# Kernel tuning notes

Measured on AMD Instinct MI355X. Metric: run time of the kernel, lower is better.

Reference implementation:

```python
import jax, jax.numpy as jnp
import numpy as np
import math

B, S, D, H, DFF, L = 8, 1024, 512, 8, 2048, 4
DK = D // H
EPS = 1e-5
NEG = -1e32


def _sinusoidal_pe(s, d):
    pos = np.arange(s)[:, None].astype(np.float32)
    div = np.exp(np.arange(0, d, 2).astype(np.float32) * (-math.log(10000.0) / d))
    pe = np.zeros((s, d), np.float32)
    pe[:, 0::2] = np.sin(pos * div)
    pe[:, 1::2] = np.cos(pos * div)
    return jnp.asarray(pe)


def setup_inputs() -> dict:
    key = jax.random.key(0)
    ks = jax.random.split(key, 20)
    sd = 0.02
    inp = {
        "q_embed_data": jax.random.normal(ks[0], (B, S, D), jnp.float32),
        "qa_embed_data": jax.random.normal(ks[1], (B, S, D), jnp.float32),
        "pe": _sinusoidal_pe(S, D),
        # stacked per-layer params (leading dim L). kq_same=1 -> q uses Wk.
        "Wk": sd * jax.random.normal(ks[2], (L, D, D), jnp.float32),
        "bk": jnp.zeros((L, D), jnp.float32),
        "Wv": sd * jax.random.normal(ks[3], (L, D, D), jnp.float32),
        "bv": jnp.zeros((L, D), jnp.float32),
        "Wo": sd * jax.random.normal(ks[4], (L, D, D), jnp.float32),
        "bo": jnp.zeros((L, D), jnp.float32),
        "ln1_s": jnp.ones((L, D), jnp.float32),
        "ln1_b": jnp.zeros((L, D), jnp.float32),
        "W1": sd * jax.random.normal(ks[5], (L, D, DFF), jnp.float32),
        "b1": jnp.zeros((L, DFF), jnp.float32),
        "W2": sd * jax.random.normal(ks[6], (L, DFF, D), jnp.float32),
        "b2": jnp.zeros((L, D), jnp.float32),
        "ln2_s": jnp.ones((L, D), jnp.float32),
        "ln2_b": jnp.zeros((L, D), jnp.float32),
    }
    return inp


def _layernorm(z, s, b):
    m = z.mean(-1, keepdims=True)
    v = ((z - m) ** 2).mean(-1, keepdims=True)
    return (z - m) / jnp.sqrt(v + EPS) * s + b


def _forward(q_embed_data, qa_embed_data, pe, Wk, bk, Wv, bv, Wo, bo,
             ln1_s, ln1_b, W1, b1, W2, b2, ln2_s, ln2_b):
    x = q_embed_data + pe[None, :, :]
    y = qa_embed_data + pe[None, :, :]  # values source stays fixed across blocks
    allowed = jnp.tril(jnp.ones((S, S), bool), -1)  # strictly-causal: attend only to j < i
    row_keep = (jnp.arange(S) > 0).astype(x.dtype)[None, None, :, None]  # zero_pad row 0

    def heads(z, W, b):
        return (z @ W + b).reshape(B, S, H, DK).transpose(0, 2, 1, 3)  # [B,H,S,DK]

    def step(xc, p):
        wk, bk_, wv, bv_, wo, bo_, s1, b1n, w1, b1f, w2, b2f, s2, b2n = p
        q = heads(xc, wk, bk_)  # kq_same: q via k_linear
        k = heads(xc, wk, bk_)
        v = heads(y, wv, bv_)
        sc = jnp.einsum('bhid,bhjd->bhij', q, k) / math.sqrt(DK)
        att = jax.nn.softmax(jnp.where(allowed, sc, NEG), axis=-1) * row_keep
        o = jnp.einsum('bhij,bhjd->bhid', att, v).transpose(0, 2, 1, 3).reshape(B, S, D)
        x1 = _layernorm(xc + (o @ wo + bo_), s1, b1n)
        f = jax.nn.relu(x1 @ w1 + b1f) @ w2 + b2f
        x2 = _layernorm(x1 + f, s2, b2n)
        return x2, None

    out, _ = jax.lax.scan(step, x, (Wk, bk, Wv, bv, Wo, bo, ln1_s, ln1_b, W1, b1, W2, b2, ln2_s, ln2_b))
    return out


def reference(q_embed_data, qa_embed_data, pe, Wk, bk, Wv, bv, Wo, bo,
              ln1_s, ln1_b, W1, b1, W2, b2, ln2_s, ln2_b):
    return _forward(q_embed_data, qa_embed_data, pe, Wk, bk, Wv, bv, Wo, bo,
                    ln1_s, ln1_b, W1, b1, W2, b2, ln2_s, ln2_b)
```

## Files before the change

kernel.cpp:

```cpp
#include <hip/hip_runtime.h>
#include <stdint.h>

typedef __attribute__((ext_vector_type(8))) __bf16 bf16x8;
typedef __attribute__((ext_vector_type(4))) float f32x4;
typedef __attribute__((ext_vector_type(4))) unsigned int u32x4;

constexpr int B = 8, S = 1024, D = 512, H = 8, DFF = 2048, L = 4, DK = 64;
constexpr int MR = B * S;

__device__ __forceinline__ unsigned short f2bf(float f) {
    union { float f; unsigned u; } v; v.f = f;
    unsigned u = v.u;
    u += 0x7fffu + ((u >> 16) & 1u);
    return (unsigned short)(u >> 16);
}

__device__ __forceinline__ void gload_lds16(const void* g, void* l) {
    __builtin_amdgcn_global_load_lds(
        (const __attribute__((address_space(1))) void*)g,
        (__attribute__((address_space(3))) void*)l, 16, 0, 0);
}

__global__ __launch_bounds__(256) void add_pe_kernel(
    const float* __restrict__ qe, const float* __restrict__ qa,
    const float* __restrict__ pe, float* __restrict__ x_f32,
    unsigned short* __restrict__ x_bf, unsigned short* __restrict__ y_bf) {
    int gid = blockIdx.x * 256 + threadIdx.x;
    int base = gid * 4;
    int po = base & (S * D - 1);
    float4 p = *(const float4*)(pe + po);
    float4 a = *(const float4*)(qe + base);
    float4 q = *(const float4*)(qa + base);
    float4 xv = make_float4(a.x + p.x, a.y + p.y, a.z + p.z, a.w + p.w);
    float4 yv = make_float4(q.x + p.x, q.y + p.y, q.z + p.z, q.w + p.w);
    *(float4*)(x_f32 + base) = xv;
    ushort4 xb; xb.x = f2bf(xv.x); xb.y = f2bf(xv.y); xb.z = f2bf(xv.z); xb.w = f2bf(xv.w);
    ushort4 yb; yb.x = f2bf(yv.x); yb.y = f2bf(yv.y); yb.z = f2bf(yv.z); yb.w = f2bf(yv.w);
    *(ushort4*)(x_bf + base) = xb;
    *(ushort4*)(y_bf + base) = yb;
}

__global__ __launch_bounds__(256) void wtrans_kernel(
    const float* __restrict__ src, unsigned short* __restrict__ dst, int K, int N) {
    __shared__ float t[64][65];
    src += (size_t)blockIdx.z * K * N;
    dst += (size_t)blockIdx.z * K * N;
    int n0 = blockIdx.x * 64, k0 = blockIdx.y * 64;
    int tid = threadIdx.x;
    int r = tid >> 4, c4 = (tid & 15) * 4;
    #pragma unroll
    for (int rr = 0; rr < 64; rr += 16) {
        float4 v = *(const float4*)(src + (size_t)(k0 + r + rr) * N + n0 + c4);
        t[r + rr][c4] = v.x; t[r + rr][c4 + 1] = v.y;
        t[r + rr][c4 + 2] = v.z; t[r + rr][c4 + 3] = v.w;
    }
    __syncthreads();
    int n = tid >> 2, kc = (tid & 3) * 16;
    ushort4 o[4];
    #pragma unroll
    for (int g = 0; g < 4; g++) {
        o[g].x = f2bf(t[kc + g * 4 + 0][n]);
        o[g].y = f2bf(t[kc + g * 4 + 1][n]);
        o[g].z = f2bf(t[kc + g * 4 + 2][n]);
        o[g].w = f2bf(t[kc + g * 4 + 3][n]);
    }
    unsigned short* dp = dst + (size_t)(n0 + n) * K + k0 + kc;
    #pragma unroll
    for (int g = 0; g < 4; g++) *(ushort4*)(dp + g * 4) = o[g];
}

template<int BN, bool RELU, bool RESID, bool OUT_F32, bool OUT_BF16, bool OUT_VT, bool BOUNCE>
__global__ __launch_bounds__(256) void gemm_kernel(
    const unsigned short* __restrict__ A, const unsigned short* __restrict__ Bt,
    const float* __restrict__ bias, const float* __restrict__ resid,
    float* __restrict__ out_f32, unsigned short* __restrict__ out_bf,
    int M, int N, int K) {
    constexpr int MT = (BN == 128) ? 4 : 2;
    constexpr int WROWS = (BN == 128) ? 64 : 32;
    constexpr int BRND = (BN == 128) ? 4 : 2;
    __shared__ unsigned short lds[(128 + BN) * 64];
    unsigned short* a_lds = lds;
    unsigned short* b_lds = lds + 128 * 64;

    const int tid = threadIdx.x;
    const int lane = tid & 63, wid = tid >> 6;
    const int wm = (BN == 128) ? (wid >> 1) : wid;
    const int wn = (BN == 128) ? (wid & 1) : 0;
    const int l15 = lane & 15, quad = lane >> 4;
    const int nmt = gridDim.x, nnt = gridDim.y;
    const int o_lin = blockIdx.y * nmt + blockIdx.x;
    const int xcd = o_lin & 7, oi = o_lin >> 3;
    const int mtile = xcd * (nmt >> 3) + oi / nnt;
    const int ntile = oi % nnt;
    const int m0 = mtile * 128, n0 = ntile * BN;

    f32x4 acc[MT][4];
    #pragma unroll
    for (int i = 0; i < MT; i++)
        #pragma unroll
        for (int j = 0; j < 4; j++) { f32x4 z = {0.f, 0.f, 0.f, 0.f}; acc[i][j] = z; }

    const unsigned short* aP[4];
    unsigned short* aL[4];
    #pragma unroll
    for (int j = 0; j < 4; j++) {
        int c = wid * 256 + j * 64 + lane;
        int r = c >> 3, slot = c & 7, kg = slot ^ (r & 7);
        aP[j] = A + (size_t)(m0 + r) * K + kg * 8;
        aL[j] = a_lds + (size_t)(wid * 256 + j * 64) * 8;
    }
    const unsigned short* bP[BRND];
    unsigned short* bL[BRND];
    #pragma unroll
    for (int j = 0; j < BRND; j++) {
        int c = wid * (BRND * 64) + j * 64 + lane;
        int r = c >> 3, slot = c & 7, kg = slot ^ (r & 7);
        bP[j] = Bt + (size_t)(n0 + r) * K + kg * 8;
        bL[j] = b_lds + (size_t)(wid * (BRND * 64) + j * 64) * 8;
    }

    for (int k0 = 0; k0 < K; k0 += 64) {
        #pragma unroll
        for (int j = 0; j < 4; j++) gload_lds16(aP[j] + k0, aL[j]);
        #pragma unroll
        for (int j = 0; j < BRND; j++) gload_lds16(bP[j] + k0, bL[j]);
        __syncthreads();

        bf16x8 af[MT][2], bfv[4][2];
        #pragma unroll
        for (int mt = 0; mt < MT; mt++) {
            int row = wm * WROWS + mt * 16 + l15;
            #pragma unroll
            for (int kh = 0; kh < 2; kh++)
                af[mt][kh] = *(const bf16x8*)&a_lds[row * 64 + (((kh * 4 + quad) ^ (row & 7)) * 8)];
        }
        #pragma unroll
        for (int nt = 0; nt < 4; nt++) {
            int row = wn * 64 + nt * 16 + l15;
            #pragma unroll
            for (int kh = 0; kh < 2; kh++)
                bfv[nt][kh] = *(const bf16x8*)&b_lds[row * 64 + (((kh * 4 + quad) ^ (row & 7)) * 8)];
        }
        #pragma unroll
        for (int mt = 0; mt < MT; mt++)
            #pragma unroll
            for (int nt = 0; nt < 4; nt++) {
                acc[mt][nt] = __builtin_amdgcn_mfma_f32_16x16x32_bf16(af[mt][0], bfv[nt][0], acc[mt][nt], 0, 0, 0);
                acc[mt][nt] = __builtin_amdgcn_mfma_f32_16x16x32_bf16(af[mt][1], bfv[nt][1], acc[mt][nt], 0, 0, 0);
            }
        __syncthreads();
    }

    if constexpr (BOUNCE) {
        float* sc = (float*)lds + wid * (16 * 68);
        const int cbase = n0 + wn * 64;
        const int r2 = lane >> 2;
        const int c2 = (lane & 3) * 16;
        float4 bvv[4];
        #pragma unroll
        for (int i = 0; i < 4; i++) bvv[i] = *(const float4*)(bias + cbase + c2 + i * 4);
        #pragma unroll
        for (int mt = 0; mt < MT; mt++) {
            #pragma unroll
            for (int nt = 0; nt < 4; nt++)
                #pragma unroll
                for (int r = 0; r < 4; r++)
                    sc[(quad * 4 + r) * 68 + nt * 16 + l15] = acc[mt][nt][r];
            const int row_g = m0 + wm * WROWS + mt * 16 + r2;
            float v[16];
            #pragma unroll
            for (int i = 0; i < 4; i++) {
                float4 t = *(const float4*)&sc[r2 * 68 + c2 + i * 4];
                v[i * 4 + 0] = t.x + bvv[i].x; v[i * 4 + 1] = t.y + bvv[i].y;
                v[i * 4 + 2] = t.z + bvv[i].z; v[i * 4 + 3] = t.w + bvv[i].w;
            }
            if (RELU) {
                #pragma unroll
                for (int i = 0; i < 16; i++) v[i] = fmaxf(v[i], 0.f);
            }
            unsigned short ob[16];
            #pragma unroll
            for (int i = 0; i < 16; i++) ob[i] = f2bf(v[i]);
            unsigned short* op = out_bf + (size_t)row_g * N + cbase + c2;
            *(u32x4*)op = *(const u32x4*)ob;
            *(u32x4*)(op + 8) = *(const u32x4*)(ob + 8);
        }
    } else {
        #pragma unroll
        for (int nt = 0; nt < 4; nt++) {
            int col = n0 + wn * 64 + nt * 16 + l15;
            float bv = bias[col];
            #pragma unroll
            for (int mt = 0; mt < MT; mt++) {
                int row0 = m0 + wm * WROWS + mt * 16 + quad * 4;
                if (OUT_VT) {
                    int hh = col >> 6, d = col & 63;
                    int bb = row0 >> 10, s0 = row0 & 1023;
                    ushort4 o;
                    o.x = f2bf(acc[mt][nt][0] + bv);
                    o.y = f2bf(acc[mt][nt][1] + bv);
                    o.z = f2bf(acc[mt][nt][2] + bv);
                    o.w = f2bf(acc[mt][nt][3] + bv);
                    *(ushort4*)(out_bf + ((size_t)(bb * H + hh) * DK + d) * S + s0) = o;
                } else {
                    #pragma unroll
                    for (int r = 0; r < 4; r++) {
                        int row = row0 + r;
                        float v = acc[mt][nt][r] + bv;
                        if (RESID) v += resid[(size_t)row * N + col];
                        if (RELU) v = fmaxf(v, 0.f);
                        size_t o = (size_t)row * N + col;
                        if (OUT_F32) out_f32[o] = v;
                        if (OUT_BF16) out_bf[o] = f2bf(v);
                    }
                }
            }
        }
    }
}

__global__ __launch_bounds__(256) void gemm_qkv_kernel(
    const unsigned short* __restrict__ x_bf, const unsigned short* __restrict__ y_bf,
    const unsigned short* __restrict__ wkT, const unsigned short* __restrict__ wvT,
    const float* __restrict__ bk, const float* __restrict__ bv,
    unsigned short* __restrict__ qk_out, unsigned short* __restrict__ vt_out) {
    constexpr int BN = 64, MT = 2, WROWS = 32, BRND = 2;
    constexpr int N = 512, K = 512;
    __shared__ unsigned short a_lds[128 * 64];
    __shared__ unsigned short b_lds[BN * 64];

    const bool isv = blockIdx.z != 0;
    const unsigned short* A  = isv ? y_bf : x_bf;
    const unsigned short* Bt = isv ? wvT : wkT;
    const float* bias        = isv ? bv : bk;

    const int tid = threadIdx.x;
    const int lane = tid & 63, wid = tid >> 6;
    const int l15 = lane & 15, quad = lane >> 4;
    const int nmt = gridDim.x, nnt = gridDim.y;
    const int o_lin = blockIdx.y * nmt + blockIdx.x;
    const int xcd = o_lin & 7, oi = o_lin >> 3;
    const int mtile = xcd * (nmt >> 3) + oi / nnt;
    const int ntile = oi % nnt;
    const int m0 = mtile * 128, n0 = ntile * BN;

    f32x4 acc[MT][4];
    #pragma unroll
    for (int i = 0; i < MT; i++)
        #pragma unroll
        for (int j = 0; j < 4; j++) { f32x4 z = {0.f, 0.f, 0.f, 0.f}; acc[i][j] = z; }

    const unsigned short* aP[4];
    unsigned short* aL[4];
    #pragma unroll
    for (int j = 0; j < 4; j++) {
        int c = wid * 256 + j * 64 + lane;
        int r = c >> 3, slot = c & 7, kg = slot ^ (r & 7);
        aP[j] = A + (size_t)(m0 + r) * K + kg * 8;
        aL[j] = a_lds + (size_t)(wid * 256 + j * 64) * 8;
    }
    const unsigned short* bP[BRND];
    unsigned short* bL[BRND];
    #pragma unroll
    for (int j = 0; j < BRND; j++) {
        int c = wid * (BRND * 64) + j * 64 + lane;
        int r = c >> 3, slot = c & 7, kg = slot ^ (r & 7);
        bP[j] = Bt + (size_t)(n0 + r) * K + kg * 8;
        bL[j] = b_lds + (size_t)(wid * (BRND * 64) + j * 64) * 8;
    }

    for (int k0 = 0; k0 < K; k0 += 64) {
        #pragma unroll
        for (int j = 0; j < 4; j++) gload_lds16(aP[j] + k0, aL[j]);
        #pragma unroll
        for (int j = 0; j < BRND; j++) gload_lds16(bP[j] + k0, bL[j]);
        __syncthreads();

        bf16x8 af[MT][2], bfv[4][2];
        #pragma unroll
        for (int mt = 0; mt < MT; mt++) {
            int row = wid * WROWS + mt * 16 + l15;
            #pragma unroll
            for (int kh = 0; kh < 2; kh++)
                af[mt][kh] = *(const bf16x8*)&a_lds[row * 64 + (((kh * 4 + quad) ^ (row & 7)) * 8)];
        }
        #pragma unroll
        for (int nt = 0; nt < 4; nt++) {
            int row = nt * 16 + l15;
            #pragma unroll
            for (int kh = 0; kh < 2; kh++)
                bfv[nt][kh] = *(const bf16x8*)&b_lds[row * 64 + (((kh * 4 + quad) ^ (row & 7)) * 8)];
        }
        #pragma unroll
        for (int mt = 0; mt < MT; mt++)
            #pragma unroll
            for (int nt = 0; nt < 4; nt++) {
                acc[mt][nt] = __builtin_amdgcn_mfma_f32_16x16x32_bf16(af[mt][0], bfv[nt][0], acc[mt][nt], 0, 0, 0);
                acc[mt][nt] = __builtin_amdgcn_mfma_f32_16x16x32_bf16(af[mt][1], bfv[nt][1], acc[mt][nt], 0, 0, 0);
            }
        __syncthreads();
    }

    #pragma unroll
    for (int nt = 0; nt < 4; nt++) {
        int col = n0 + nt * 16 + l15;
        float bv_ = bias[col];
        #pragma unroll
        for (int mt = 0; mt < MT; mt++) {
            int row0 = m0 + wid * WROWS + mt * 16 + quad * 4;
            ushort4 o;
            o.x = f2bf(acc[mt][nt][0] + bv_);
            o.y = f2bf(acc[mt][nt][1] + bv_);
            o.z = f2bf(acc[mt][nt][2] + bv_);
            o.w = f2bf(acc[mt][nt][3] + bv_);
            if (isv) {
                int hh = col >> 6, d = col & 63;
                int bb = row0 >> 10, s0 = row0 & 1023;
                *(ushort4*)(vt_out + ((size_t)(bb * H + hh) * DK + d) * S + s0) = o;
            } else {
                #pragma unroll
                for (int r = 0; r < 4; r++)
                    qk_out[(size_t)(row0 + r) * N + col] =
                        (r == 0) ? o.x : (r == 1) ? o.y : (r == 2) ? o.z : o.w;
            }
        }
    }
}

__global__ __launch_bounds__(256) void ln_kernel(
    const float* __restrict__ in, const float* __restrict__ gamma,
    const float* __restrict__ beta, float* __restrict__ out_f32,
    unsigned short* __restrict__ out_bf) {
    __shared__ float red[8];
    int row = blockIdx.x, tid = threadIdx.x;
    const float* p = in + (size_t)row * D;
    float2 v = *(const float2*)(p + tid * 2);
    float s = v.x + v.y;
    float q = v.x * v.x + v.y * v.y;
    #pragma unroll
    for (int off = 32; off > 0; off >>= 1) {
        s += __shfl_xor(s, off);
        q += __shfl_xor(q, off);
    }
    int wid = tid >> 6, lane = tid & 63;
    if (lane == 0) { red[wid] = s; red[4 + wid] = q; }
    __syncthreads();
    s = red[0] + red[1] + red[2] + red[3];
    q = red[4] + red[5] + red[6] + red[7];
    float mean = s * (1.f / D);
    float var = q * (1.f / D) - mean * mean;
    float inv = rsqrtf(var + 1e-5f);
    int c = tid * 2;
    float2 g = *(const float2*)(gamma + c);
    float2 bb = *(const float2*)(beta + c);
    float o0 = (v.x - mean) * inv * g.x + bb.x;
    float o1 = (v.y - mean) * inv * g.y + bb.y;
    *(float2*)(out_f32 + (size_t)row * D + c) = make_float2(o0, o1);
    ushort2 ob; ob.x = f2bf(o0); ob.y = f2bf(o1);
    *(ushort2*)(out_bf + (size_t)row * D + c) = ob;
}

__global__ __launch_bounds__(256, 2) void attn_kernel(
    const unsigned short* __restrict__ qk, const unsigned short* __restrict__ vt,
    unsigned short* __restrict__ ob) {
    __shared__ unsigned short kbuf[2][64 * 64];
    __shared__ unsigned short vbuf[2][64 * 64];
    __shared__ unsigned p_u32[4][32 * 36];
    constexpr float C = 0.18033688011112042f;
    const float NEGINF = -__builtin_huge_valf();

    const int bx = blockIdx.x;
    const int Qb = 7 - (bx >> 6);
    const int hh = bx & 63;
    const int b = hh >> 3, h = hh & 7;
    const int head = hh;
    const int tid = threadIdx.x;
    const int w = tid >> 6, lane = tid & 63;
    const int l15 = lane & 15, quad = lane >> 4;

    const int nkt = 2 * Qb + 2;
    const int qrow0 = Qb * 128 + w * 32;

    const int rowbase = b * S, colbase = h * DK;
    const unsigned short* kbase = qk + (size_t)rowbase * D + colbase;
    const unsigned short* vbase = vt + (size_t)head * (DK * S);

    bf16x8 qf[2][2];
    #pragma unroll
    for (int u = 0; u < 2; u++) {
        const unsigned short* qrow =
            qk + (size_t)(rowbase + qrow0 + u * 16 + l15) * D + colbase;
        qf[u][0] = *(const bf16x8*)(qrow + quad * 8);
        qf[u][1] = *(const bf16x8*)(qrow + 32 + quad * 8);
    }

    const int sr = lane >> 3;
    const int sseg = (lane & 7) ^ sr;
    const unsigned short* kgp[2]; const unsigned short* vgp[2];
    unsigned short* kld[2]; unsigned short* vld[2];
    #pragma unroll
    for (int j = 0; j < 2; j++) {
        int rt = w * 16 + j * 8 + sr;
        kgp[j] = kbase + (size_t)rt * D + sseg * 8;
        vgp[j] = vbase + (size_t)rt * S + sseg * 8;
        kld[j] = &kbuf[0][(w * 16 + j * 8) * 64];
        vld[j] = &vbuf[0][(w * 16 + j * 8) * 64];
    }
    auto stage = [&](int buf, int kt) {
        #pragma unroll
        for (int j = 0; j < 2; j++) gload_lds16(kgp[j] + (size_t)kt * 64 * D, kld[j] + buf * 4096);
        #pragma unroll
        for (int j = 0; j < 2; j++) gload_lds16(vgp[j] + kt * 64, vld[j] + buf * 4096);
    };

    float l_r[2] = {0.f, 0.f};
    f32x4 o_acc[2][4];
    #pragma unroll
    for (int u = 0; u < 2; u++)
        #pragma unroll
        for (int i = 0; i < 4; i++) { f32x4 z = {0.f, 0.f, 0.f, 0.f}; o_acc[u][i] = z; }

    auto consume = [&](int kt, const unsigned short* kl, const unsigned short* vl) {
        unsigned* pb = p_u32[w];
        bf16x8 kf[4][2];
        #pragma unroll
        for (int mt = 0; mt < 4; mt++) {
            const unsigned short* kr = kl + (mt * 16 + l15) * 64;
            #pragma unroll
            for (int kh = 0; kh < 2; kh++)
                kf[mt][kh] = *(const bf16x8*)(kr + (((kh * 4 + quad) ^ (l15 & 7)) * 8));
        }
        const bool diag = kt * 64 + 64 > qrow0;
        #pragma unroll
        for (int u = 0; u < 2; u++) {
            const int qb = qrow0 + u * 16;
            const int ql = u * 16 + l15;
            #pragma unroll
            for (int mt = 0; mt < 4; mt++) {
                if (kt * 64 + mt * 16 < qb + 16) {
                    f32x4 a = {0.f, 0.f, 0.f, 0.f};
                    a = __builtin_amdgcn_mfma_f32_16x16x32_bf16(kf[mt][0], qf[u][0], a, 0, 0, 0);
                    a = __builtin_amdgcn_mfma_f32_16x16x32_bf16(kf[mt][1], qf[u][1], a, 0, 0, 0);
                    if (diag) {
                        const int gi = qb + l15;
                        #pragma unroll
                        for (int r = 0; r < 4; r++) {
                            int gj = kt * 64 + mt * 16 + quad * 4 + r;
                            a[r] = (gj >= gi) ? NEGINF : a[r];
                        }
                    }
                    float e0 = exp2f(a[0] * C), e1 = exp2f(a[1] * C);
                    float e2 = exp2f(a[2] * C), e3 = exp2f(a[3] * C);
                    unsigned pk0, pk1;
                    asm("v_cvt_pk_bf16_f32 %0, %1, %2" : "=v"(pk0) : "v"(e0), "v"(e1));
                    asm("v_cvt_pk_bf16_f32 %0, %1, %2" : "=v"(pk1) : "v"(e2), "v"(e3));
                    l_r[u] += (e0 + e1) + (e2 + e3);
                    *(uint2*)&pb[ql * 36 + mt * 8 + quad * 2] = make_uint2(pk0, pk1);
                } else {
                    *(uint2*)&pb[ql * 36 + mt * 8 + quad * 2] = make_uint2(0u, 0u);
                }
            }
        }
        bf16x8 vf[4][2];
        #pragma unroll
        for (int mt = 0; mt < 4; mt++) {
            const unsigned short* vr = vl + (mt * 16 + l15) * 64;
            #pragma unroll
            for (int kh = 0; kh < 2; kh++)
                vf[mt][kh] = *(const bf16x8*)(vr + (((kh * 4 + quad) ^ (l15 & 7)) * 8));
        }
        #pragma unroll
        for (int u = 0; u < 2; u++) {
            const int qb = qrow0 + u * 16;
            const int ql = u * 16 + l15;
            u32x4 d0 = *(const u32x4*)&pb[ql * 36 + quad * 4];
            bf16x8 pb0 = __builtin_bit_cast(bf16x8, d0);
            const bool hi = (kt * 64 + 32 < qb + 16);
            if (hi) {
                u32x4 d1 = *(const u32x4*)&pb[ql * 36 + 16 + quad * 4];
                bf16x8 pb1 = __builtin_bit_cast(bf16x8, d1);
                #pragma unroll
                for (int mt = 0; mt < 4; mt++) {
                    o_acc[u][mt] = __builtin_amdgcn_mfma_f32_16x16x32_bf16(vf[mt][0], pb0, o_acc[u][mt], 0, 0, 0);
                    o_acc[u][mt] = __builtin_amdgcn_mfma_f32_16x16x32_bf16(vf[mt][1], pb1, o_acc[u][mt], 0, 0, 0);
                }
            } else {
                #pragma unroll
                for (int mt = 0; mt < 4; mt++)
                    o_acc[u][mt] = __builtin_amdgcn_mfma_f32_16x16x32_bf16(vf[mt][0], pb0, o_acc[u][mt], 0, 0, 0);
            }
        }
    };

    stage(0, 0);
    for (int kt = 0; kt < nkt; ++kt) {
        const int cur = kt & 1;
        if (kt + 1 < nkt) {
            stage(cur ^ 1, kt + 1);
            asm volatile("s_waitcnt vmcnt(4)" ::: "memory");
        } else {
            asm volatile("s_waitcnt vmcnt(0)" ::: "memory");
        }
        __builtin_amdgcn_sched_barrier(0);
        __builtin_amdgcn_s_barrier();
        __builtin_amdgcn_sched_barrier(0);
        if (kt * 64 < qrow0 + 32)
            consume(kt, &kbuf[cur][0], &vbuf[cur][0]);
        __builtin_amdgcn_sched_barrier(0);
        __builtin_amdgcn_s_barrier();
        __builtin_amdgcn_sched_barrier(0);
    }

    #pragma unroll
    for (int u = 0; u < 2; u++) {
        l_r[u] += __shfl_xor(l_r[u], 16);
        l_r[u] += __shfl_xor(l_r[u], 32);
    }
    #pragma unroll
    for (int u = 0; u < 2; u++) {
        const int si = qrow0 + u * 16 + l15;
        float inv = (l_r[u] > 0.f) ? 1.f / l_r[u] : 0.f;
        if (si == 0) inv = 0.f;
        unsigned short* orow = ob + (size_t)(b * S + si) * D + h * DK;
        #pragma unroll
        for (int mt = 0; mt < 4; mt++) {
            ushort4 o;
            o.x = f2bf(o_acc[u][mt][0] * inv);
            o.y = f2bf(o_acc[u][mt][1] * inv);
            o.z = f2bf(o_acc[u][mt][2] * inv);
            o.w = f2bf(o_acc[u][mt][3] * inv);
            *(ushort4*)(orow + mt * 16 + quad * 4) = o;
        }
    }
}

extern "C" void kernel_launch(void* const* d_in, const int* in_sizes, int n_in,
                              void* d_out, int out_size, void* d_ws, size_t ws_size,
                              hipStream_t stream) {
    (void)in_sizes; (void)n_in; (void)out_size; (void)ws_size;
    const float* qe  = (const float*)d_in[0];
    const float* qa  = (const float*)d_in[1];
    const float* pe  = (const float*)d_in[2];
    const float* Wk  = (const float*)d_in[3];
    const float* bk  = (const float*)d_in[4];
    const float* Wv  = (const float*)d_in[5];
    const float* bv  = (const float*)d_in[6];
    const float* Wo  = (const float*)d_in[7];
    const float* bo  = (const float*)d_in[8];
    const float* l1s = (const float*)d_in[9];
    const float* l1b = (const float*)d_in[10];
    const float* W1  = (const float*)d_in[11];
    const float* b1  = (const float*)d_in[12];
    const float* W2  = (const float*)d_in[13];
    const float* b2  = (const float*)d_in[14];
    const float* l2s = (const float*)d_in[15];
    const float* l2b = (const float*)d_in[16];

    char* w = (char*)d_ws;
    float* x_f32  = (float*)w;           w += (size_t)MR * D * 4;
    float* t_f32  = (float*)w;           w += (size_t)MR * D * 4;
    float* x1_f32 = (float*)w;           w += (size_t)MR * D * 4;
    unsigned short* x_bf  = (unsigned short*)w; w += (size_t)MR * D * 2;
    unsigned short* y_bf  = (unsigned short*)w; w += (size_t)MR * D * 2;
    unsigned short* qk_bf = (unsigned short*)w; w += (size_t)MR * D * 2;
    unsigned short* vt_bf = (unsigned short*)w; w += (size_t)MR * D * 2;
    unsigned short* o_bf  = (unsigned short*)w; w += (size_t)MR * D * 2;
    unsigned short* x1_bf = (unsigned short*)w; w += (size_t)MR * D * 2;
    unsigned short* h_bf  = (unsigned short*)w; w += (size_t)MR * DFF * 2;
    unsigned short* wkT = (unsigned short*)w;   w += (size_t)L * D * D * 2;
    unsigned short* wvT = (unsigned short*)w;   w += (size_t)L * D * D * 2;
    unsigned short* woT = (unsigned short*)w;   w += (size_t)L * D * D * 2;
    unsigned short* w1T = (unsigned short*)w;   w += (size_t)L * D * DFF * 2;
    unsigned short* w2T = (unsigned short*)w;   w += (size_t)L * DFF * D * 2;

    add_pe_kernel<<<MR * D / 4 / 256, 256, 0, stream>>>(qe, qa, pe, x_f32, x_bf, y_bf);
    wtrans_kernel<<<dim3(8, 8, L), 256, 0, stream>>>(Wk, wkT, D, D);
    wtrans_kernel<<<dim3(8, 8, L), 256, 0, stream>>>(Wv, wvT, D, D);
    wtrans_kernel<<<dim3(8, 8, L), 256, 0, stream>>>(Wo, woT, D, D);
    wtrans_kernel<<<dim3(32, 8, L), 256, 0, stream>>>(W1, w1T, D, DFF);
    wtrans_kernel<<<dim3(8, 32, L), 256, 0, stream>>>(W2, w2T, DFF, D);

    dim3 g512(64, 8), g2048(64, 16);
    for (int l = 0; l < L; l++) {
        gemm_qkv_kernel<<<dim3(64, 8, 2), 256, 0, stream>>>(
            x_bf, y_bf, wkT + (size_t)l * D * D, wvT + (size_t)l * D * D,
            bk + l * D, bv + l * D, qk_bf, vt_bf);
        attn_kernel<<<512, 256, 0, stream>>>(qk_bf, vt_bf, o_bf);
        gemm_kernel<64, false, true, true, false, false, false><<<g512, 256, 0, stream>>>(
            o_bf, woT + (size_t)l * D * D, bo + l * D, x_f32, t_f32, nullptr, MR, D, D);
        ln_kernel<<<MR, 256, 0, stream>>>(t_f32, l1s + l * D, l1b + l * D, x1_f32, x1_bf);
        gemm_kernel<128, true, false, false, true, false, true><<<g2048, 256, 0, stream>>>(
            x1_bf, w1T + (size_t)l * D * DFF, b1 + l * DFF, nullptr, nullptr, h_bf, MR, DFF, D);
        gemm_kernel<64, false, true, true, false, false, false><<<g512, 256, 0, stream>>>(
            h_bf, w2T + (size_t)l * DFF * D, b2 + l * D, x1_f32, t_f32, nullptr, MR, D, DFF);
        float* xo = (l == L - 1) ? (float*)d_out : x_f32;
        ln_kernel<<<MR, 256, 0, stream>>>(t_f32, l2s + l * D, l2b + l * D, xo, x_bf);
    }
}
```

Measured before the change: 710.0 us.

## Add dedicated 256x256-tile FFN1 GEMM kernel with ping-pong LDS pipelining

Replaces the generic 128x128-tile gemm used for the FFN up-projection (x1 @ W1 + b1, ReLU) with a specialized 512-thread kernel. The new kernel uses 256x256 output tiles, a double-buffered LDS that is refilled via global_load_lds while MFMAs run, phase barriers with setprio, and XCD-aware tile remapping. The goal is higher data reuse per loaded tile and better overlap of memory loads with compute for the largest GEMM. In exchange it needs 128KB of LDS, which limits occupancy, and launches a grid of only 256 blocks, which may leave compute units underused. The BOUNCE epilogue path is removed from the generic gemm and kept only in the new kernel.

```diff
diff --git a/kernel.cpp b/kernel.cpp
--- a/kernel.cpp
+++ b/kernel.cpp
@@ -69,7 +69,7 @@
     for (int g = 0; g < 4; g++) *(ushort4*)(dp + g * 4) = o[g];
 }
 
-template<int BN, bool RELU, bool RESID, bool OUT_F32, bool OUT_BF16, bool OUT_VT, bool BOUNCE>
+template<int BN, bool RELU, bool RESID, bool OUT_F32, bool OUT_BF16, bool OUT_VT>
 __global__ __launch_bounds__(256) void gemm_kernel(
     const unsigned short* __restrict__ A, const unsigned short* __restrict__ Bt,
     const float* __restrict__ bias, const float* __restrict__ resid,
@@ -151,71 +151,166 @@
         __syncthreads();
     }
 
-    if constexpr (BOUNCE) {
-        float* sc = (float*)lds + wid * (16 * 68);
-        const int cbase = n0 + wn * 64;
-        const int r2 = lane >> 2;
-        const int c2 = (lane & 3) * 16;
-        float4 bvv[4];
-        #pragma unroll
-        for (int i = 0; i < 4; i++) bvv[i] = *(const float4*)(bias + cbase + c2 + i * 4);
+    #pragma unroll
+    for (int nt = 0; nt < 4; nt++) {
+        int col = n0 + wn * 64 + nt * 16 + l15;
+        float bv = bias[col];
         #pragma unroll
         for (int mt = 0; mt < MT; mt++) {
-            #pragma unroll
-            for (int nt = 0; nt < 4; nt++)
+            int row0 = m0 + wm * WROWS + mt * 16 + quad * 4;
+            if (OUT_VT) {
+                int hh = col >> 6, d = col & 63;
+                int bb = row0 >> 10, s0 = row0 & 1023;
+                ushort4 o;
+                o.x = f2bf(acc[mt][nt][0] + bv);
+                o.y = f2bf(acc[mt][nt][1] + bv);
+                o.z = f2bf(acc[mt][nt][2] + bv);
+                o.w = f2bf(acc[mt][nt][3] + bv);
+                *(ushort4*)(out_bf + ((size_t)(bb * H + hh) * DK + d) * S + s0) = o;
+            } else {
                 #pragma unroll
-                for (int r = 0; r < 4; r++)
-                    sc[(quad * 4 + r) * 68 + nt * 16 + l15] = acc[mt][nt][r];
-            const int row_g = m0 + wm * WROWS + mt * 16 + r2;
-            float v[16];
-            #pragma unroll
-            for (int i = 0; i < 4; i++) {
-                float4 t = *(const float4*)&sc[r2 * 68 + c2 + i * 4];
-                v[i * 4 + 0] = t.x + bvv[i].x; v[i * 4 + 1] = t.y + bvv[i].y;
-                v[i * 4 + 2] = t.z + bvv[i].z; v[i * 4 + 3] = t.w + bvv[i].w;
-            }
-            if (RELU) {
+                for (int r = 0; r < 4; r++) {
+                    int row = row0 + r;
+                    float v = acc[mt][nt][r] + bv;
+                    if (RESID) v += resid[(size_t)row * N + col];
+                    if (RELU) v = fmaxf(v, 0.f);
+                    size_t o = (size_t)row * N + col;
+                    if (OUT_F32) out_f32[o] = v;
+                    if (OUT_BF16) out_bf[o] = f2bf(v);
+                }
+            }
+        }
+    }
+}
+
+__global__ __launch_bounds__(512, 2) void ffn1_kernel(
+    const unsigned short* __restrict__ A, const unsigned short* __restrict__ Bt,
+    const float* __restrict__ bias, unsigned short* __restrict__ out_bf) {
+    constexpr int K = 512, N = 2048;
+    __shared__ unsigned short lds[2 * 32768];
+
+    const int tid = threadIdx.x;
+    const int lane = tid & 63, w = tid >> 6;
+    const int wm = w >> 2, wn = w & 3;
+    const int l15 = lane & 15, quad = lane >> 4;
+    const int nmt = gridDim.x, nnt = gridDim.y;
+    const int o_lin = blockIdx.y * nmt + blockIdx.x;
+    const int xcd = o_lin & 7, oi = o_lin >> 3;
+    const int mtile = xcd * (nmt >> 3) + oi / nnt;
+    const int ntile = oi % nnt;
+    const int m0 = mtile * 256, n0 = ntile * 256;
+
+    f32x4 acc[8][4];
+    #pragma unroll
+    for (int i = 0; i < 8; i++)
+        #pragma unroll
+        for (int j = 0; j < 4; j++) { f32x4 z = {0.f, 0.f, 0.f, 0.f}; acc[i][j] = z; }
+
+    const unsigned short* gp[4][2];
+    unsigned short* lp[4][2];
+    #pragma unroll
+    for (int h = 0; h < 4; h++)
+        #pragma unroll
+        for (int j = 0; j < 2; j++) {
+            int c = j * 512 + tid;
+            int r = c >> 3, s = c & 7, kg = s ^ (r & 7);
+            const unsigned short* base = (h < 2)
+                ? A + (size_t)(m0 + h * 128 + r) * K
+                : Bt + (size_t)(n0 + (h - 2) * 128 + r) * K;
+            gp[h][j] = base + kg * 8;
+            lp[h][j] = lds + h * 8192 + (size_t)(j * 512 + w * 64) * 8;
+        }
+    auto stage_half = [&](int buf, int kt, int h) {
+        #pragma unroll
+        for (int j = 0; j < 2; j++)
+            gload_lds16(gp[h][j] + kt * 64, lp[h][j] + buf * 32768);
+    };
+
+    #pragma unroll
+    for (int h = 0; h < 4; h++) stage_half(0, 0, h);
+    asm volatile("s_waitcnt vmcnt(0)" ::: "memory");
+    __builtin_amdgcn_sched_barrier(0);
+    __builtin_amdgcn_s_barrier();
+    __builtin_amdgcn_sched_barrier(0);
+
+    for (int kt = 0; kt < 8; ++kt) {
+        const int cur = kt & 1;
+        const unsigned short* ab = lds + cur * 32768;
+        const unsigned short* bb = ab + 16384;
+        bf16x8 bf[4][2];
+        #pragma unroll
+        for (int p = 0; p < 4; p++) {
+            if (kt < 7) stage_half(cur ^ 1, kt + 1, p);
+            if (p == 0) {
                 #pragma unroll
-                for (int i = 0; i < 16; i++) v[i] = fmaxf(v[i], 0.f);
-            }
-            unsigned short ob[16];
-            #pragma unroll
-            for (int i = 0; i < 16; i++) ob[i] = f2bf(v[i]);
-            unsigned short* op = out_bf + (size_t)row_g * N + cbase + c2;
-            *(u32x4*)op = *(const u32x4*)ob;
-            *(u32x4*)(op + 8) = *(const u32x4*)(ob + 8);
-        }
-    } else {
-        #pragma unroll
-        for (int nt = 0; nt < 4; nt++) {
-            int col = n0 + wn * 64 + nt * 16 + l15;
-            float bv = bias[col];
-            #pragma unroll
-            for (int mt = 0; mt < MT; mt++) {
-                int row0 = m0 + wm * WROWS + mt * 16 + quad * 4;
-                if (OUT_VT) {
-                    int hh = col >> 6, d = col & 63;
-                    int bb = row0 >> 10, s0 = row0 & 1023;
-                    ushort4 o;
-                    o.x = f2bf(acc[mt][nt][0] + bv);
-                    o.y = f2bf(acc[mt][nt][1] + bv);
-                    o.z = f2bf(acc[mt][nt][2] + bv);
-                    o.w = f2bf(acc[mt][nt][3] + bv);
-                    *(ushort4*)(out_bf + ((size_t)(bb * H + hh) * DK + d) * S + s0) = o;
-                } else {
+                for (int nf = 0; nf < 4; nf++) {
+                    int rowb = wn * 64 + nf * 16 + l15;
                     #pragma unroll
-                    for (int r = 0; r < 4; r++) {
-                        int row = row0 + r;
-                        float v = acc[mt][nt][r] + bv;
-                        if (RESID) v += resid[(size_t)row * N + col];
-                        if (RELU) v = fmaxf(v, 0.f);
-                        size_t o = (size_t)row * N + col;
-                        if (OUT_F32) out_f32[o] = v;
-                        if (OUT_BF16) out_bf[o] = f2bf(v);
-                    }
+                    for (int kh = 0; kh < 2; kh++)
+                        bf[nf][kh] = *(const bf16x8*)&bb[rowb * 64 + (((kh * 4 + quad) ^ (rowb & 7)) * 8)];
                 }
             }
-        }
+            bf16x8 af[2][2];
+            #pragma unroll
+            for (int f = 0; f < 2; f++) {
+                int row = wm * 128 + (2 * p + f) * 16 + l15;
+                #pragma unroll
+                for (int kh = 0; kh < 2; kh++)
+                    af[f][kh] = *(const bf16x8*)&ab[row * 64 + (((kh * 4 + quad) ^ (row & 7)) * 8)];
+            }
+            __builtin_amdgcn_s_barrier();
+            asm volatile("s_waitcnt lgkmcnt(0)" ::: "memory");
+            __builtin_amdgcn_sched_barrier(0);
+            __builtin_amdgcn_s_setprio(1);
+            #pragma unroll
+            for (int f = 0; f < 2; f++)
+                #pragma unroll
+                for (int nf = 0; nf < 4; nf++) {
+                    acc[2 * p + f][nf] = __builtin_amdgcn_mfma_f32_16x16x32_bf16(af[f][0], bf[nf][0], acc[2 * p + f][nf], 0, 0, 0);
+                    acc[2 * p + f][nf] = __builtin_amdgcn_mfma_f32_16x16x32_bf16(af[f][1], bf[nf][1], acc[2 * p + f][nf], 0, 0, 0);
+                }
+            __builtin_amdgcn_s_setprio(0);
+            if (p < 3) {
+                __builtin_amdgcn_sched_barrier(0);
+                __builtin_amdgcn_s_barrier();
+                __builtin_amdgcn_sched_barrier(0);
+            }
+        }
+        asm volatile("s_waitcnt vmcnt(0)" ::: "memory");
+        __builtin_amdgcn_sched_barrier(0);
+        __builtin_amdgcn_s_barrier();
+        __builtin_amdgcn_sched_barrier(0);
+    }
+
+    float* sc = (float*)lds + w * (16 * 68);
+    const int cbase = n0 + wn * 64;
+    const int r2 = lane >> 2, c2 = (lane & 3) * 16;
+    float4 bvv[4];
+    #pragma unroll
+    for (int i = 0; i < 4; i++) bvv[i] = *(const float4*)(bias + cbase + c2 + i * 4);
+    #pragma unroll
+    for (int mt = 0; mt < 8; mt++) {
+        #pragma unroll
+        for (int nt = 0; nt < 4; nt++)
+            #pragma unroll
+            for (int r = 0; r < 4; r++)
+                sc[(quad * 4 + r) * 68 + nt * 16 + l15] = acc[mt][nt][r];
+        const int row_g = m0 + wm * 128 + mt * 16 + r2;
+        float v[16];
+        #pragma unroll
+        for (int i = 0; i < 4; i++) {
+            float4 t = *(const float4*)&sc[r2 * 68 + c2 + i * 4];
+            v[i * 4 + 0] = fmaxf(t.x + bvv[i].x, 0.f);
+            v[i * 4 + 1] = fmaxf(t.y + bvv[i].y, 0.f);
+            v[i * 4 + 2] = fmaxf(t.z + bvv[i].z, 0.f);
+            v[i * 4 + 3] = fmaxf(t.w + bvv[i].w, 0.f);
+        }
+        unsigned short ob[16];
+        #pragma unroll
+        for (int i = 0; i < 16; i++) ob[i] = f2bf(v[i]);
+        unsigned short* op = out_bf + (size_t)row_g * N + cbase + c2;
+        *(u32x4*)op = *(const u32x4*)ob;
+        *(u32x4*)(op + 8) = *(const u32x4*)(ob + 8);
     }
 }
 
@@ -580,18 +675,18 @@
     wtrans_kernel<<<dim3(32, 8, L), 256, 0, stream>>>(W1, w1T, D, DFF);
     wtrans_kernel<<<dim3(8, 32, L), 256, 0, stream>>>(W2, w2T, DFF, D);
 
-    dim3 g512(64, 8), g2048(64, 16);
+    dim3 g512(64, 8);
     for (int l = 0; l < L; l++) {
         gemm_qkv_kernel<<<dim3(64, 8, 2), 256, 0, stream>>>(
             x_bf, y_bf, wkT + (size_t)l * D * D, wvT + (size_t)l * D * D,
             bk + l * D, bv + l * D, qk_bf, vt_bf);
         attn_kernel<<<512, 256, 0, stream>>>(qk_bf, vt_bf, o_bf);
-        gemm_kernel<64, false, true, true, false, false, false><<<g512, 256, 0, stream>>>(
+        gemm_kernel<64, false, true, true, false, false><<<g512, 256, 0, stream>>>(
             o_bf, woT + (size_t)l * D * D, bo + l * D, x_f32, t_f32, nullptr, MR, D, D);
         ln_kernel<<<MR, 256, 0, stream>>>(t_f32, l1s + l * D, l1b + l * D, x1_f32, x1_bf);
-        gemm_kernel<128, true, false, false, true, false, true><<<g2048, 256, 0, stream>>>(
-            x1_bf, w1T + (size_t)l * D * DFF, b1 + l * DFF, nullptr, nullptr, h_bf, MR, DFF, D);
-        gemm_kernel<64, false, true, true, false, false, false><<<g512, 256, 0, stream>>>(
+        ffn1_kernel<<<dim3(32, 8), 512, 0, stream>>>(
+            x1_bf, w1T + (size_t)l * D * DFF, b1 + l * DFF, h_bf);
+        gemm_kernel<64, false, true, true, false, false><<<g512, 256, 0, stream>>>(
             h_bf, w2T + (size_t)l * DFF * D, b2 + l * D, x1_f32, t_f32, nullptr, MR, D, DFF);
         float* xo = (l == L - 1) ? (float*)d_out : x_f32;
         ln_kernel<<<MR, 256, 0, stream>>>(t_f32, l2s + l * D, l2b + l * D, xo, x_bf);
```

Measured after the change: 731.1 us. 1.03x slower.
